# Kernel tuning notes

Measured on AMD Instinct MI355X. Metric: run time of the kernel, lower is better.

The kernel has to match this reference:

```python
import jax, jax.numpy as jnp
import numpy as np

T, B, H = 512, 256, 256


def setup_inputs() -> dict:
    key = jax.random.key(0)
    k1, k2, k3, k4 = jax.random.split(key, 4)
    ins = jax.random.normal(k1, (T, B, H), jnp.float32)
    resets = jax.random.randint(k2, (T, B), 0, 2) > 0  # bool reset mask
    carry = jnp.zeros((B, H), jnp.float32)
    scale = 1.0 / np.sqrt(H).astype(np.float32)
    # Fused GRU weights: columns ordered [r | z | n] for input and hidden projections.
    Wi = jax.random.normal(k3, (H, 3 * H), jnp.float32) * scale  # dense_i kernels (ir, iz, in)
    Wh = jax.random.normal(k4, (H, 3 * H), jnp.float32) * scale  # dense_h kernels (hr, hz, hn)
    bi = jnp.zeros((3 * H,), jnp.float32)   # dense_i biases (ir, iz, in)
    bhn = jnp.zeros((H,), jnp.float32)      # dense_h bias, only the 'hn' gate has one in flax GRUCell
    return dict(ins=ins, resets=resets, carry=carry, Wi=Wi, bi=bi, Wh=Wh, bhn=bhn)


def reference(ins, resets, carry, Wi, bi, Wh, bhn):
    """Faithful jax version of ScannedRNN: per-step reset-masked flax GRUCell scan.

    flax GRUCell math:
      r = sigmoid(x@Wir + bir + h@Whr)
      z = sigmoid(x@Wiz + biz + h@Whz)
      n = tanh(x@Win + bin + r * (h@Whn + bhn))
      h' = (1-z)*n + z*h ; output y = h'
    Reset mask zeroes the carry before the cell (initialize_carry -> zeros).
    """
    def step(h, xt):
        x, reset = xt  # x: [B,H], reset: [B]
        h = jnp.where(reset[:, None], jnp.zeros_like(h), h)
        gi = x @ Wi + bi          # [B, 3H]
        gh = h @ Wh               # [B, 3H]
        ir_, iz_, in_ = jnp.split(gi, 3, axis=-1)
        hr_, hz_, hn_ = jnp.split(gh, 3, axis=-1)
        r = jax.nn.sigmoid(ir_ + hr_)
        z = jax.nn.sigmoid(iz_ + hz_)
        n = jnp.tanh(in_ + r * (hn_ + bhn))
        h_new = (1.0 - z) * n + z * h
        return h_new, h_new

    _, ys = jax.lax.scan(step, carry, (ins, resets))
    return ys  # [T, B, H]
```

## Files before the change

kernel.cpp:

```cpp
#include <hip/hip_runtime.h>
#include <stdint.h>


typedef __attribute__((ext_vector_type(8))) __bf16 bf16x8;
typedef __attribute__((ext_vector_type(4))) float f32x4;

__device__ __forceinline__ float bf2f(unsigned short u) {
    union { unsigned int i; float f; } v; v.i = ((unsigned int)u) << 16; return v.f;
}
__device__ __forceinline__ unsigned short f2bf(float f) {
    union { float f; unsigned int i; } v; v.f = f;
    unsigned int x = v.i;
    x = x + 0x7fffu + ((x >> 16) & 1u);
    return (unsigned short)(x >> 16);
}
__device__ __forceinline__ float fsig(float x) {
    return __builtin_amdgcn_rcpf(1.f + __builtin_amdgcn_exp2f(-1.442695041f * x));
}
__device__ __forceinline__ float ftanh(float x) {
    return 1.f - 2.f * __builtin_amdgcn_rcpf(1.f + __builtin_amdgcn_exp2f(2.885390082f * x));
}

__global__ void prep_weights(const float* __restrict__ Wi, const float* __restrict__ Wh,
                             unsigned short* __restrict__ WiT, unsigned short* __restrict__ WhT) {
    const int idx = blockIdx.x * 256 + threadIdx.x;
    const float* src = blockIdx.y ? Wh : Wi;
    unsigned short* dst = blockIdx.y ? WhT : WiT;
    const int c = idx >> 8, k = idx & 255;
    dst[c * 256 + k] = f2bf(src[k * 768 + c]);
}

__launch_bounds__(512, 2)
__global__ void gi_gemm(const float* __restrict__ ins, const unsigned short* __restrict__ WiT,
                        const float* __restrict__ bi, unsigned short* __restrict__ GI) {
    __shared__ unsigned short a_buf[16 * 264];
    __shared__ float gi_stage[16 * 776];

    const int tid = threadIdx.x;
    const int lane = tid & 63, wv = tid >> 6;
    const int quad = lane >> 4, n16 = lane & 15;

    bf16x8 wfrag[3][2][8];
#pragma unroll
    for (int g = 0; g < 3; ++g)
#pragma unroll
        for (int tl = 0; tl < 2; ++tl) {
            const int c = g * 256 + wv * 32 + tl * 16 + n16;
            const unsigned short* src = WiT + c * 256 + quad * 8;
#pragma unroll
            for (int kt = 0; kt < 8; ++kt)
                wfrag[g][tl][kt] = *(const bf16x8*)(src + kt * 32);
        }
    float bi_r[3][2];
#pragma unroll
    for (int g = 0; g < 3; ++g)
#pragma unroll
        for (int tl = 0; tl < 2; ++tl)
            bi_r[g][tl] = bi[g * 256 + wv * 32 + tl * 16 + n16];

    const int srow = tid >> 5;
    const int scol = (tid & 31) * 8;

    float4 p0, p1;
    {
        const float* p = ins + (size_t)blockIdx.x * 16 * 256 + tid * 8;
        p0 = *(const float4*)p; p1 = *(const float4*)(p + 4);
    }

    for (int i = 0; i < 32; ++i) {
        const int chunk = blockIdx.x + i * 256;
        {
            bf16x8 av;
            av[0] = (__bf16)p0.x; av[1] = (__bf16)p0.y; av[2] = (__bf16)p0.z; av[3] = (__bf16)p0.w;
            av[4] = (__bf16)p1.x; av[5] = (__bf16)p1.y; av[6] = (__bf16)p1.z; av[7] = (__bf16)p1.w;
            *(bf16x8*)(&a_buf[srow * 264 + scol]) = av;
        }
        if (i + 1 < 32) {
            const float* p = ins + (size_t)(blockIdx.x + (i + 1) * 256) * 16 * 256 + tid * 8;
            p0 = *(const float4*)p; p1 = *(const float4*)(p + 4);
        }
        __syncthreads();

        f32x4 acc[3][2] = {};
#pragma unroll
        for (int kt = 0; kt < 8; ++kt) {
            bf16x8 af = *(const bf16x8*)(&a_buf[n16 * 264 + kt * 32 + quad * 8]);
#pragma unroll
            for (int g = 0; g < 3; ++g)
#pragma unroll
                for (int tl = 0; tl < 2; ++tl)
                    acc[g][tl] = __builtin_amdgcn_mfma_f32_16x16x32_bf16(af, wfrag[g][tl][kt], acc[g][tl], 0, 0, 0);
        }
#pragma unroll
        for (int g = 0; g < 3; ++g)
#pragma unroll
            for (int tl = 0; tl < 2; ++tl) {
                const int c = g * 256 + wv * 32 + tl * 16 + n16;
#pragma unroll
                for (int r = 0; r < 4; ++r)
                    gi_stage[(quad * 4 + r) * 776 + c] = acc[g][tl][r] + bi_r[g][tl];
            }
        __syncthreads();
        {
            const int r2 = tid >> 5;
            const int cb = (tid & 31) * 24;
            const int t = (chunk * 16) >> 8;
            const int b0 = (chunk * 16) & 255;
            unsigned short* dst = GI + ((size_t)(b0 + r2) * 512 + t) * 768 + cb;
            const float* sp = &gi_stage[r2 * 776 + cb];
#pragma unroll
            for (int u = 0; u < 3; ++u) {
                bf16x8 o;
#pragma unroll
                for (int j = 0; j < 8; ++j) o[j] = (__bf16)sp[u * 8 + j];
                *(bf16x8*)(dst + u * 8) = o;
            }
        }
    }
}

__launch_bounds__(512, 2)
__global__ void gru_scan(const unsigned short* __restrict__ GI, const int* __restrict__ resets,
                         const float* __restrict__ carry, const unsigned short* __restrict__ WhT,
                         const float* __restrict__ bhn, float* __restrict__ out) {
    __shared__ int s_reset[512];
    __shared__ unsigned short s_h[2][16 * 264];
    __shared__ unsigned short s_gi[2][16 * 784];

    const int b = blockIdx.x;
    const int tid = threadIdx.x;
    const int lane = tid & 63, wv = tid >> 6;
    const int quad = lane >> 4, n16 = lane & 15;

    s_reset[tid] = resets[tid * 256 + b];

    bf16x8 wfrag[3][2][8];
#pragma unroll
    for (int g = 0; g < 3; ++g)
#pragma unroll
        for (int tl = 0; tl < 2; ++tl) {
            const int c = g * 256 + wv * 32 + tl * 16 + n16;
            const unsigned short* src = WhT + c * 256 + quad * 8;
#pragma unroll
            for (int kt = 0; kt < 8; ++kt)
                wfrag[g][tl][kt] = *(const bf16x8*)(src + kt * 32);
        }
    float bhn_r[2];
    bhn_r[0] = bhn[wv * 32 + n16];
    bhn_r[1] = bhn[wv * 32 + 16 + n16];

    __syncthreads();

    int t_s[4];
    float h_prev[2][4];
#pragma unroll
    for (int r = 0; r < 4; ++r) {
        const int slot = quad * 4 + r;
        const int w0 = slot * 32;
        int found = -1;
        for (int t = w0; t < w0 + 32; ++t) {
            if (t == 0 || s_reset[t] != 0) { found = t; break; }
        }
        t_s[r] = found;
        float h0 = 0.f, h1 = 0.f;
        if (found == 0 && s_reset[0] == 0) {
            h0 = carry[b * 256 + wv * 32 + n16];
            h1 = carry[b * 256 + wv * 32 + 16 + n16];
        }
        h_prev[0][r] = h0; h_prev[1][r] = h1;
        s_h[0][slot * 264 + wv * 32 + n16] = f2bf(h0);
        s_h[0][slot * 264 + wv * 32 + 16 + n16] = f2bf(h1);
    }

    int buf = 0;
    for (int it = 0; it < 513; ++it) {
        const bool any = (t_s[0] >= 0) | (t_s[1] >= 0) | (t_s[2] >= 0) | (t_s[3] >= 0);
        if (__ballot((int)any) == 0ull) break;

        {
            const int src_lane = (wv >> 1) * 16;
            const int v0 = __builtin_amdgcn_readlane(t_s[0], src_lane);
            const int v1 = __builtin_amdgcn_readlane(t_s[1], src_lane);
            const int v2 = __builtin_amdgcn_readlane(t_s[2], src_lane);
            const int v3 = __builtin_amdgcn_readlane(t_s[3], src_lane);
            const int tr0 = (wv & 1) ? v2 : v0;
            const int tr1 = (wv & 1) ? v3 : v1;
            if (tr0 >= 0) {
                const unsigned short* src = GI + ((size_t)b * 512 + tr0) * 768 + lane * 12;
                unsigned short* d = &s_gi[buf][(2 * wv) * 784 + lane * 12];
                ((uint2*)d)[0] = ((const uint2*)src)[0];
                ((uint2*)d)[1] = ((const uint2*)src)[1];
                ((uint2*)d)[2] = ((const uint2*)src)[2];
            }
            if (tr1 >= 0) {
                const unsigned short* src = GI + ((size_t)b * 512 + tr1) * 768 + lane * 12;
                unsigned short* d = &s_gi[buf][(2 * wv + 1) * 784 + lane * 12];
                ((uint2*)d)[0] = ((const uint2*)src)[0];
                ((uint2*)d)[1] = ((const uint2*)src)[1];
                ((uint2*)d)[2] = ((const uint2*)src)[2];
            }
        }
        __syncthreads();

        f32x4 acc[3][2] = {};
#pragma unroll
        for (int kt = 0; kt < 8; ++kt) {
            bf16x8 af = *(const bf16x8*)(&s_h[buf][n16 * 264 + kt * 32 + quad * 8]);
#pragma unroll
            for (int g = 0; g < 3; ++g)
#pragma unroll
                for (int tl = 0; tl < 2; ++tl)
                    acc[g][tl] = __builtin_amdgcn_mfma_f32_16x16x32_bf16(af, wfrag[g][tl][kt], acc[g][tl], 0, 0, 0);
        }

#pragma unroll
        for (int r = 0; r < 4; ++r) {
            const int slot = quad * 4 + r;
            const int t_cur = t_s[r];
            const bool alive = t_cur >= 0;
            float hnew[2];
#pragma unroll
            for (int tl = 0; tl < 2; ++tl) {
                const int c = wv * 32 + tl * 16 + n16;
                const float gr = bf2f(s_gi[buf][slot * 784 + c]);
                const float gz = bf2f(s_gi[buf][slot * 784 + 256 + c]);
                const float gn = bf2f(s_gi[buf][slot * 784 + 512 + c]);
                const float rr = fsig(gr + acc[0][tl][r]);
                const float zz = fsig(gz + acc[1][tl][r]);
                const float nn = ftanh(gn + rr * (acc[2][tl][r] + bhn_r[tl]));
                hnew[tl] = (1.f - zz) * nn + zz * h_prev[tl][r];
                if (alive) out[((size_t)t_cur * 256 + b) * 256 + c] = hnew[tl];
            }
            int tnext = -1;
            bool zero_h = true;
            if (alive) {
                const int tn = t_cur + 1;
                if (tn < 512) {
                    const bool rst = s_reset[tn] != 0;
                    if (!(rst && tn >= (slot + 1) * 32)) {
                        tnext = tn;
                        zero_h = rst;
                    }
                }
            }
            t_s[r] = tnext;
            const float k0 = zero_h ? 0.f : hnew[0];
            const float k1 = zero_h ? 0.f : hnew[1];
            h_prev[0][r] = k0; h_prev[1][r] = k1;
            s_h[buf ^ 1][slot * 264 + wv * 32 + n16] = f2bf(k0);
            s_h[buf ^ 1][slot * 264 + wv * 32 + 16 + n16] = f2bf(k1);
        }
        buf ^= 1;
    }
}

extern "C" void kernel_launch(void* const* d_in, const int* in_sizes, int n_in,
                              void* d_out, int out_size, void* d_ws, size_t ws_size,
                              hipStream_t stream) {
    const float* ins   = (const float*)d_in[0];
    const int* resets  = (const int*)d_in[1];
    const float* carry = (const float*)d_in[2];
    const float* Wi    = (const float*)d_in[3];
    const float* bi    = (const float*)d_in[4];
    const float* Wh    = (const float*)d_in[5];
    const float* bhn   = (const float*)d_in[6];
    float* out = (float*)d_out;

    unsigned short* WiT = (unsigned short*)d_ws;
    unsigned short* WhT = WiT + 196608;
    unsigned short* GI  = WhT + 196608;

    prep_weights<<<dim3(768, 2), dim3(256), 0, stream>>>(Wi, Wh, WiT, WhT);
    gi_gemm<<<dim3(256), dim3(512), 0, stream>>>(ins, WiT, bi, GI);
    gru_scan<<<dim3(256), dim3(512), 0, stream>>>(GI, resets, carry, WhT, bhn, out);
}
```

Baseline: 459.2 us.

## Retile input GEMM into 128x128 blocks and prefetch gate inputs in GRU scan

The input-projection GEMM becomes a conventional 128x128-tiled kernel over 6144 blocks, with K-chunk register prefetch and a block-id swizzle, replacing the 256-block kernel that held weights in registers. In the scan, Wh is pre-swizzled into MFMA fragment order. The hn-gate fragments move to LDS to cut register pressure, and precomputed input gates are prefetched straight into registers one step ahead instead of staged through LDS. Segment end times are now precomputed so the per-step liveness test is simpler. Together these aim to cut GEMM overhead and shorten the serial scan's critical path, at the cost of extra LDS reads per step and scattered 2-byte global loads.

```diff
diff --git a/kernel.cpp b/kernel.cpp
--- a/kernel.cpp
+++ b/kernel.cpp
@@ -22,110 +22,199 @@
 }
 
 __global__ void prep_weights(const float* __restrict__ Wi, const float* __restrict__ Wh,
-                             unsigned short* __restrict__ WiT, unsigned short* __restrict__ WhT) {
+                             unsigned short* __restrict__ WiT, unsigned short* __restrict__ WhFrag) {
     const int idx = blockIdx.x * 256 + threadIdx.x;
-    const float* src = blockIdx.y ? Wh : Wi;
-    unsigned short* dst = blockIdx.y ? WhT : WiT;
-    const int c = idx >> 8, k = idx & 255;
-    dst[c * 256 + k] = f2bf(src[k * 768 + c]);
-}
-
-__launch_bounds__(512, 2)
+    if (blockIdx.y == 0) {
+        const int c = idx >> 8, k = idx & 255;
+        WiT[c * 256 + k] = f2bf(Wi[k * 768 + c]);
+    } else {
+        const int j    = idx & 7;
+        const int lane = (idx >> 3) & 63;
+        const int fi   = (idx >> 9) % 48;
+        const int wv   = (idx >> 9) / 48;
+        const int kt = fi & 7, g2 = fi >> 3;
+        const int g = g2 >> 1, tl = g2 & 1;
+        const int quad = lane >> 4, n16 = lane & 15;
+        const int k = kt * 32 + quad * 8 + j;
+        const int c = g * 256 + wv * 32 + tl * 16 + n16;
+        WhFrag[idx] = f2bf(Wh[k * 768 + c]);
+    }
+}
+
+__launch_bounds__(256, 2)
 __global__ void gi_gemm(const float* __restrict__ ins, const unsigned short* __restrict__ WiT,
                         const float* __restrict__ bi, unsigned short* __restrict__ GI) {
-    __shared__ unsigned short a_buf[16 * 264];
-    __shared__ float gi_stage[16 * 776];
-
+    __shared__ char smem[36864];
+    unsigned short* a_t = (unsigned short*)smem;
+    unsigned short* b_t = a_t + 128 * 72;
+    float* stg = (float*)smem;
+
+    const int bid0 = blockIdx.x;
+    const int bid  = (bid0 & 7) * 768 + (bid0 >> 3);
+    const int mtile = bid / 6, ntile = bid - mtile * 6;
+    const int R0 = mtile * 128;
+    const int N0 = ntile * 128;
     const int tid = threadIdx.x;
-    const int lane = tid & 63, wv = tid >> 6;
+    const int lane = tid & 63;
+    const int wv = tid >> 6;
     const int quad = lane >> 4, n16 = lane & 15;
-
-    bf16x8 wfrag[3][2][8];
-#pragma unroll
-    for (int g = 0; g < 3; ++g)
-#pragma unroll
-        for (int tl = 0; tl < 2; ++tl) {
-            const int c = g * 256 + wv * 32 + tl * 16 + n16;
-            const unsigned short* src = WiT + c * 256 + quad * 8;
-#pragma unroll
-            for (int kt = 0; kt < 8; ++kt)
-                wfrag[g][tl][kt] = *(const bf16x8*)(src + kt * 32);
-        }
-    float bi_r[3][2];
-#pragma unroll
-    for (int g = 0; g < 3; ++g)
-#pragma unroll
-        for (int tl = 0; tl < 2; ++tl)
-            bi_r[g][tl] = bi[g * 256 + wv * 32 + tl * 16 + n16];
-
-    const int srow = tid >> 5;
-    const int scol = (tid & 31) * 8;
-
-    float4 p0, p1;
+    const int wm = wv >> 1, wn = wv & 1;
+
+    const int srow = tid >> 1;
+    const int koff = (tid & 1) * 32;
+
+    float bi_r[4];
+#pragma unroll
+    for (int nt = 0; nt < 4; ++nt) bi_r[nt] = bi[N0 + wn * 64 + nt * 16 + n16];
+
+    float4 areg[8];
+    uint4 breg[4];
     {
-        const float* p = ins + (size_t)blockIdx.x * 16 * 256 + tid * 8;
-        p0 = *(const float4*)p; p1 = *(const float4*)(p + 4);
-    }
-
-    for (int i = 0; i < 32; ++i) {
-        const int chunk = blockIdx.x + i * 256;
-        {
+        const float* ap = ins + (size_t)(R0 + srow) * 256 + koff;
+#pragma unroll
+        for (int i = 0; i < 8; ++i) areg[i] = *(const float4*)(ap + i * 4);
+        const unsigned short* bp = WiT + (size_t)(N0 + srow) * 256 + koff;
+#pragma unroll
+        for (int i = 0; i < 4; ++i) breg[i] = *(const uint4*)(bp + i * 8);
+    }
+
+    f32x4 acc[4][4] = {};
+
+    for (int kk = 0; kk < 4; ++kk) {
+        __syncthreads();
+#pragma unroll
+        for (int i = 0; i < 4; ++i) {
             bf16x8 av;
-            av[0] = (__bf16)p0.x; av[1] = (__bf16)p0.y; av[2] = (__bf16)p0.z; av[3] = (__bf16)p0.w;
-            av[4] = (__bf16)p1.x; av[5] = (__bf16)p1.y; av[6] = (__bf16)p1.z; av[7] = (__bf16)p1.w;
-            *(bf16x8*)(&a_buf[srow * 264 + scol]) = av;
-        }
-        if (i + 1 < 32) {
-            const float* p = ins + (size_t)(blockIdx.x + (i + 1) * 256) * 16 * 256 + tid * 8;
-            p0 = *(const float4*)p; p1 = *(const float4*)(p + 4);
-        }
+            const float* f = (const float*)&areg[i * 2];
+#pragma unroll
+            for (int j2 = 0; j2 < 8; ++j2) av[j2] = (__bf16)f[j2];
+            *(bf16x8*)(&a_t[srow * 72 + koff + i * 8]) = av;
+        }
+#pragma unroll
+        for (int i = 0; i < 4; ++i)
+            *(uint4*)(&b_t[srow * 72 + koff + i * 8]) = breg[i];
         __syncthreads();
-
-        f32x4 acc[3][2] = {};
-#pragma unroll
-        for (int kt = 0; kt < 8; ++kt) {
-            bf16x8 af = *(const bf16x8*)(&a_buf[n16 * 264 + kt * 32 + quad * 8]);
-#pragma unroll
-            for (int g = 0; g < 3; ++g)
-#pragma unroll
-                for (int tl = 0; tl < 2; ++tl)
-                    acc[g][tl] = __builtin_amdgcn_mfma_f32_16x16x32_bf16(af, wfrag[g][tl][kt], acc[g][tl], 0, 0, 0);
-        }
-#pragma unroll
-        for (int g = 0; g < 3; ++g)
-#pragma unroll
-            for (int tl = 0; tl < 2; ++tl) {
-                const int c = g * 256 + wv * 32 + tl * 16 + n16;
-#pragma unroll
-                for (int r = 0; r < 4; ++r)
-                    gi_stage[(quad * 4 + r) * 776 + c] = acc[g][tl][r] + bi_r[g][tl];
-            }
+        if (kk < 3) {
+            const float* ap = ins + (size_t)(R0 + srow) * 256 + (kk + 1) * 64 + koff;
+#pragma unroll
+            for (int i = 0; i < 8; ++i) areg[i] = *(const float4*)(ap + i * 4);
+            const unsigned short* bp = WiT + (size_t)(N0 + srow) * 256 + (kk + 1) * 64 + koff;
+#pragma unroll
+            for (int i = 0; i < 4; ++i) breg[i] = *(const uint4*)(bp + i * 8);
+        }
+#pragma unroll
+        for (int kt = 0; kt < 2; ++kt) {
+            bf16x8 afr[4], bfr[4];
+#pragma unroll
+            for (int mt = 0; mt < 4; ++mt)
+                afr[mt] = *(const bf16x8*)(&a_t[(wm * 64 + mt * 16 + n16) * 72 + kt * 32 + quad * 8]);
+#pragma unroll
+            for (int nt = 0; nt < 4; ++nt)
+                bfr[nt] = *(const bf16x8*)(&b_t[(wn * 64 + nt * 16 + n16) * 72 + kt * 32 + quad * 8]);
+#pragma unroll
+            for (int mt = 0; mt < 4; ++mt)
+#pragma unroll
+                for (int nt = 0; nt < 4; ++nt)
+                    acc[mt][nt] = __builtin_amdgcn_mfma_f32_16x16x32_bf16(afr[mt], bfr[nt], acc[mt][nt], 0, 0, 0);
+        }
+    }
+
+#pragma unroll
+    for (int p = 0; p < 2; ++p) {
         __syncthreads();
-        {
-            const int r2 = tid >> 5;
-            const int cb = (tid & 31) * 24;
-            const int t = (chunk * 16) >> 8;
-            const int b0 = (chunk * 16) & 255;
-            unsigned short* dst = GI + ((size_t)(b0 + r2) * 512 + t) * 768 + cb;
-            const float* sp = &gi_stage[r2 * 776 + cb];
-#pragma unroll
-            for (int u = 0; u < 3; ++u) {
-                bf16x8 o;
-#pragma unroll
-                for (int j = 0; j < 8; ++j) o[j] = (__bf16)sp[u * 8 + j];
-                *(bf16x8*)(dst + u * 8) = o;
-            }
-        }
-    }
-}
+        if (wm == p) {
+#pragma unroll
+            for (int mt = 0; mt < 4; ++mt)
+#pragma unroll
+                for (int nt = 0; nt < 4; ++nt)
+#pragma unroll
+                    for (int r = 0; r < 4; ++r)
+                        stg[(mt * 16 + quad * 4 + r) * 132 + wn * 64 + nt * 16 + n16] = acc[mt][nt][r] + bi_r[nt];
+        }
+        __syncthreads();
+        const int row = tid >> 2, c0 = (tid & 3) * 32;
+        const int grow = R0 + p * 64 + row;
+        const int tg = grow >> 8, bg = grow & 255;
+        unsigned short* dst = GI + ((size_t)bg * 512 + tg) * 768 + N0 + c0;
+        const float* sp = &stg[row * 132 + c0];
+#pragma unroll
+        for (int u = 0; u < 4; ++u) {
+            bf16x8 o;
+#pragma unroll
+            for (int j2 = 0; j2 < 8; ++j2) o[j2] = (__bf16)sp[u * 8 + j2];
+            *(bf16x8*)(dst + u * 8) = o;
+        }
+    }
+}
+
+
+#define SCAN_STEP(GCUR, GNXT)                                                                   \
+    {                                                                                           \
+        const bool any_ = (t_cur[0] <= t_end[0]) | (t_cur[1] <= t_end[1]) |                     \
+                          (t_cur[2] <= t_end[2]) | (t_cur[3] <= t_end[3]);                      \
+        if (__ballot((int)any_) == 0ull) break;                                                 \
+        __syncthreads();                                                                        \
+        f32x4 acc2[6] = {};                                                                     \
+        _Pragma("unroll")                                                                       \
+        for (int kt = 0; kt < 8; ++kt) {                                                        \
+            bf16x8 af = *(const bf16x8*)(&s_h[buf][n16 * 264 + kt * 32 + quad * 8]);            \
+            _Pragma("unroll")                                                                   \
+            for (int g2 = 0; g2 < 4; ++g2)                                                      \
+                acc2[g2] = __builtin_amdgcn_mfma_f32_16x16x32_bf16(af, wfr[g2][kt], acc2[g2], 0, 0, 0); \
+            _Pragma("unroll")                                                                   \
+            for (int tl = 0; tl < 2; ++tl) {                                                    \
+                bf16x8 bfn = *(const bf16x8*)(&s_whn[(wv * 16 + tl * 8 + kt) * 512 + lane * 8]); \
+                acc2[4 + tl] = __builtin_amdgcn_mfma_f32_16x16x32_bf16(af, bfn, acc2[4 + tl], 0, 0, 0); \
+            }                                                                                   \
+        }                                                                                       \
+        _Pragma("unroll")                                                                       \
+        for (int r = 0; r < 4; ++r) {                                                           \
+            const int trn = (t_cur[r] < t_end[r]) ? (t_cur[r] + 1) : 0;                         \
+            const unsigned short* gp = GI + gibase + (size_t)trn * 768;                         \
+            GNXT[r][0] = gp[0];   GNXT[r][1] = gp[16];                                          \
+            GNXT[r][2] = gp[256]; GNXT[r][3] = gp[272];                                         \
+            GNXT[r][4] = gp[512]; GNXT[r][5] = gp[528];                                         \
+        }                                                                                       \
+        float hn[2][4];                                                                         \
+        _Pragma("unroll")                                                                       \
+        for (int r = 0; r < 4; ++r) {                                                           \
+            const bool alive = t_cur[r] <= t_end[r];                                            \
+            _Pragma("unroll")                                                                   \
+            for (int tl = 0; tl < 2; ++tl) {                                                    \
+                const int c = wv * 32 + tl * 16 + n16;                                          \
+                const float gr = bf2f(GCUR[r][tl]);                                             \
+                const float gz = bf2f(GCUR[r][2 + tl]);                                         \
+                const float gn = bf2f(GCUR[r][4 + tl]);                                         \
+                const float rr = fsig(gr + acc2[tl][r]);                                        \
+                const float zz = fsig(gz + acc2[2 + tl][r]);                                    \
+                const float nn = ftanh(gn + rr * (acc2[4 + tl][r] + bhn_r[tl]));                \
+                hn[tl][r] = (1.f - zz) * nn + zz * h_prev[tl][r];                               \
+                if (alive) out[((size_t)t_cur[r] * 256 + b) * 256 + c] = hn[tl][r];             \
+            }                                                                                   \
+        }                                                                                       \
+        _Pragma("unroll")                                                                       \
+        for (int r = 0; r < 4; ++r) {                                                           \
+            const int slot = quad * 4 + r;                                                      \
+            const bool alive = t_cur[r] <= t_end[r];                                            \
+            const int tn = t_cur[r] + 1;                                                        \
+            const bool nalive = alive && (tn <= t_end[r]);                                      \
+            float k0 = 0.f, k1 = 0.f;                                                           \
+            if (nalive && s_reset[tn] == 0) { k0 = hn[0][r]; k1 = hn[1][r]; }                   \
+            h_prev[0][r] = k0; h_prev[1][r] = k1;                                               \
+            s_h[buf ^ 1][slot * 264 + wv * 32 + n16] = f2bf(k0);                                \
+            s_h[buf ^ 1][slot * 264 + wv * 32 + 16 + n16] = f2bf(k1);                           \
+            if (alive) t_cur[r] = tn;                                                           \
+        }                                                                                       \
+        buf ^= 1;                                                                               \
+    }
 
 __launch_bounds__(512, 2)
 __global__ void gru_scan(const unsigned short* __restrict__ GI, const int* __restrict__ resets,
-                         const float* __restrict__ carry, const unsigned short* __restrict__ WhT,
+                         const float* __restrict__ carry, const unsigned short* __restrict__ WhFrag,
                          const float* __restrict__ bhn, float* __restrict__ out) {
     __shared__ int s_reset[512];
     __shared__ unsigned short s_h[2][16 * 264];
-    __shared__ unsigned short s_gi[2][16 * 784];
+    __shared__ unsigned short s_whn[8 * 16 * 512];
 
     const int b = blockIdx.x;
     const int tid = threadIdx.x;
@@ -134,123 +223,63 @@
 
     s_reset[tid] = resets[tid * 256 + b];
 
-    bf16x8 wfrag[3][2][8];
-#pragma unroll
-    for (int g = 0; g < 3; ++g)
-#pragma unroll
-        for (int tl = 0; tl < 2; ++tl) {
-            const int c = g * 256 + wv * 32 + tl * 16 + n16;
-            const unsigned short* src = WhT + c * 256 + quad * 8;
-#pragma unroll
-            for (int kt = 0; kt < 8; ++kt)
-                wfrag[g][tl][kt] = *(const bf16x8*)(src + kt * 32);
-        }
+    const unsigned short* wfbase = WhFrag + (size_t)wv * 48 * 512 + lane * 8;
+    bf16x8 wfr[4][8];
+#pragma unroll
+    for (int g2 = 0; g2 < 4; ++g2)
+#pragma unroll
+        for (int kt = 0; kt < 8; ++kt)
+            wfr[g2][kt] = *(const bf16x8*)(wfbase + (g2 * 8 + kt) * 512);
+#pragma unroll
+    for (int j2 = 0; j2 < 16; ++j2) {
+        bf16x8 v = *(const bf16x8*)(wfbase + (32 + j2) * 512);
+        *(bf16x8*)(&s_whn[(wv * 16 + j2) * 512 + lane * 8]) = v;
+    }
     float bhn_r[2];
     bhn_r[0] = bhn[wv * 32 + n16];
     bhn_r[1] = bhn[wv * 32 + 16 + n16];
 
     __syncthreads();
 
-    int t_s[4];
+    int t_cur[4], t_end[4];
     float h_prev[2][4];
 #pragma unroll
     for (int r = 0; r < 4; ++r) {
         const int slot = quad * 4 + r;
         const int w0 = slot * 32;
-        int found = -1;
-        for (int t = w0; t < w0 + 32; ++t) {
-            if (t == 0 || s_reset[t] != 0) { found = t; break; }
-        }
-        t_s[r] = found;
+        int st = -1;
+        for (int t = w0; t < w0 + 32; ++t)
+            if (t == 0 || s_reset[t] != 0) { st = t; break; }
+        int en = 511;
+        for (int t = w0 + 32; t < 512; ++t)
+            if (s_reset[t] != 0) { en = t - 1; break; }
         float h0 = 0.f, h1 = 0.f;
-        if (found == 0 && s_reset[0] == 0) {
+        if (st == 0 && s_reset[0] == 0) {
             h0 = carry[b * 256 + wv * 32 + n16];
             h1 = carry[b * 256 + wv * 32 + 16 + n16];
         }
+        if (st < 0) { t_cur[r] = 1; t_end[r] = 0; }
+        else        { t_cur[r] = st; t_end[r] = en; }
         h_prev[0][r] = h0; h_prev[1][r] = h1;
         s_h[0][slot * 264 + wv * 32 + n16] = f2bf(h0);
         s_h[0][slot * 264 + wv * 32 + 16 + n16] = f2bf(h1);
     }
 
+    const size_t gibase = (size_t)b * 512 * 768 + (size_t)(wv * 32 + n16);
+    unsigned short gva[4][6], gvb[4][6];
+#pragma unroll
+    for (int r = 0; r < 4; ++r) {
+        const int tr0 = (t_cur[r] <= t_end[r]) ? t_cur[r] : 0;
+        const unsigned short* gp = GI + gibase + (size_t)tr0 * 768;
+        gva[r][0] = gp[0];   gva[r][1] = gp[16];
+        gva[r][2] = gp[256]; gva[r][3] = gp[272];
+        gva[r][4] = gp[512]; gva[r][5] = gp[528];
+    }
+
     int buf = 0;
-    for (int it = 0; it < 513; ++it) {
-        const bool any = (t_s[0] >= 0) | (t_s[1] >= 0) | (t_s[2] >= 0) | (t_s[3] >= 0);
-        if (__ballot((int)any) == 0ull) break;
-
-        {
-            const int src_lane = (wv >> 1) * 16;
-            const int v0 = __builtin_amdgcn_readlane(t_s[0], src_lane);
-            const int v1 = __builtin_amdgcn_readlane(t_s[1], src_lane);
-            const int v2 = __builtin_amdgcn_readlane(t_s[2], src_lane);
-            const int v3 = __builtin_amdgcn_readlane(t_s[3], src_lane);
-            const int tr0 = (wv & 1) ? v2 : v0;
-            const int tr1 = (wv & 1) ? v3 : v1;
-            if (tr0 >= 0) {
-                const unsigned short* src = GI + ((size_t)b * 512 + tr0) * 768 + lane * 12;
-                unsigned short* d = &s_gi[buf][(2 * wv) * 784 + lane * 12];
-                ((uint2*)d)[0] = ((const uint2*)src)[0];
-                ((uint2*)d)[1] = ((const uint2*)src)[1];
-                ((uint2*)d)[2] = ((const uint2*)src)[2];
-            }
-            if (tr1 >= 0) {
-                const unsigned short* src = GI + ((size_t)b * 512 + tr1) * 768 + lane * 12;
-                unsigned short* d = &s_gi[buf][(2 * wv + 1) * 784 + lane * 12];
-                ((uint2*)d)[0] = ((const uint2*)src)[0];
-                ((uint2*)d)[1] = ((const uint2*)src)[1];
-                ((uint2*)d)[2] = ((const uint2*)src)[2];
-            }
-        }
-        __syncthreads();
-
-        f32x4 acc[3][2] = {};
-#pragma unroll
-        for (int kt = 0; kt < 8; ++kt) {
-            bf16x8 af = *(const bf16x8*)(&s_h[buf][n16 * 264 + kt * 32 + quad * 8]);
-#pragma unroll
-            for (int g = 0; g < 3; ++g)
-#pragma unroll
-                for (int tl = 0; tl < 2; ++tl)
-                    acc[g][tl] = __builtin_amdgcn_mfma_f32_16x16x32_bf16(af, wfrag[g][tl][kt], acc[g][tl], 0, 0, 0);
-        }
-
-#pragma unroll
-        for (int r = 0; r < 4; ++r) {
-            const int slot = quad * 4 + r;
-            const int t_cur = t_s[r];
-            const bool alive = t_cur >= 0;
-            float hnew[2];
-#pragma unroll
-            for (int tl = 0; tl < 2; ++tl) {
-                const int c = wv * 32 + tl * 16 + n16;
-                const float gr = bf2f(s_gi[buf][slot * 784 + c]);
-                const float gz = bf2f(s_gi[buf][slot * 784 + 256 + c]);
-                const float gn = bf2f(s_gi[buf][slot * 784 + 512 + c]);
-                const float rr = fsig(gr + acc[0][tl][r]);
-                const float zz = fsig(gz + acc[1][tl][r]);
-                const float nn = ftanh(gn + rr * (acc[2][tl][r] + bhn_r[tl]));
-                hnew[tl] = (1.f - zz) * nn + zz * h_prev[tl][r];
-                if (alive) out[((size_t)t_cur * 256 + b) * 256 + c] = hnew[tl];
-            }
-            int tnext = -1;
-            bool zero_h = true;
-            if (alive) {
-                const int tn = t_cur + 1;
-                if (tn < 512) {
-                    const bool rst = s_reset[tn] != 0;
-                    if (!(rst && tn >= (slot + 1) * 32)) {
-                        tnext = tn;
-                        zero_h = rst;
-                    }
-                }
-            }
-            t_s[r] = tnext;
-            const float k0 = zero_h ? 0.f : hnew[0];
-            const float k1 = zero_h ? 0.f : hnew[1];
-            h_prev[0][r] = k0; h_prev[1][r] = k1;
-            s_h[buf ^ 1][slot * 264 + wv * 32 + n16] = f2bf(k0);
-            s_h[buf ^ 1][slot * 264 + wv * 32 + 16 + n16] = f2bf(k1);
-        }
-        buf ^= 1;
+    for (int it2 = 0; it2 < 256; ++it2) {
+        SCAN_STEP(gva, gvb)
+        SCAN_STEP(gvb, gva)
     }
 }
 
@@ -266,11 +295,11 @@
     const float* bhn   = (const float*)d_in[6];
     float* out = (float*)d_out;
 
-    unsigned short* WiT = (unsigned short*)d_ws;
-    unsigned short* WhT = WiT + 196608;
-    unsigned short* GI  = WhT + 196608;
-
-    prep_weights<<<dim3(768, 2), dim3(256), 0, stream>>>(Wi, Wh, WiT, WhT);
-    gi_gemm<<<dim3(256), dim3(512), 0, stream>>>(ins, WiT, bi, GI);
-    gru_scan<<<dim3(256), dim3(512), 0, stream>>>(GI, resets, carry, WhT, bhn, out);
-}
+    unsigned short* WiT    = (unsigned short*)d_ws;
+    unsigned short* WhFrag = WiT + 196608;
+    unsigned short* GI     = WhFrag + 196608;
+
+    prep_weights<<<dim3(768, 2), dim3(256), 0, stream>>>(Wi, Wh, WiT, WhFrag);
+    gi_gemm<<<dim3(6144), dim3(256), 0, stream>>>(ins, WiT, bi, GI);
+    gru_scan<<<dim3(256), dim3(512), 0, stream>>>(GI, resets, carry, WhFrag, bhn, out);
+}
```

After: 590.0 us. +28.5%, slower.
